# Kernel optimization log

Hardware: AMD Instinct MI355X
Metric: run time of the kernel (lower is better)

The kernel has to match this reference:

```python
import jax, jax.numpy as jnp
import numpy as np

N, E, F, K, T = 100000, 1600000, 64, 3, 2
EPS = 1e-5


def gcn_norm(row, col, edge_weight, num_nodes):
    # symmetric normalization WITHOUT self loops (PyG ARMAConv behavior)
    deg = jax.ops.segment_sum(edge_weight, col, num_segments=num_nodes)
    dis = jnp.where(deg > 0, jax.lax.rsqrt(deg), 0.0)
    return dis[row] * edge_weight * dis[col]


def arma_conv(x, row, col, norm, init_w, w, root_w, bias, num_nodes):
    # x: [N, Fin]; init_w: [K, Fin, Fout]; w: [K, T-1, Fout, Fout]
    # root_w: [K, T, Fin, Fout]; bias: [K, T, 1, Fout]
    n_layers = root_w.shape[1]
    out = jnp.einsum('nf,kfo->kno', x, init_w)  # [K, N, Fout]
    for t in range(n_layers):
        if t > 0:
            out = jnp.einsum('kno,kop->knp', out, w[:, t - 1])
        msg = out[:, row, :] * norm[None, :, None]  # [K, E, Fout]
        out = jax.vmap(lambda m: jax.ops.segment_sum(m, col, num_segments=num_nodes))(msg)
        out = out + jnp.einsum('nf,kfo->kno', x, root_w[:, t]) + bias[:, t]
        out = jax.nn.relu(out)  # ARMAConv act between layers and at output
    return out.mean(axis=0)  # mean over stacks -> [N, Fout]


def batchnorm(h, gamma, beta):
    mu = h.mean(axis=0)
    var = h.var(axis=0)
    return gamma * (h - mu) * jax.lax.rsqrt(var + EPS) + beta


def setup_inputs() -> dict:
    key = jax.random.key(0)
    ks = jax.random.split(key, 16)
    inp = {}
    inp['x'] = jax.random.normal(ks[0], (N, F), jnp.float32)
    inp['edge_index'] = jax.random.randint(ks[1], (2, E), 0, N, dtype=jnp.int32)
    inp['weights'] = jax.random.uniform(ks[2], (E,), jnp.float32)
    s = 0.1
    i = 3
    for c in (1, 2, 3):
        inp[f'iw{c}'] = jax.random.normal(ks[i], (K, F, F), jnp.float32) * s; i += 1
        inp[f'w{c}'] = jax.random.normal(ks[i], (K, T - 1, F, F), jnp.float32) * s; i += 1
        inp[f'rw{c}'] = jax.random.normal(ks[i], (K, T, F, F), jnp.float32) * s; i += 1
        inp[f'b{c}'] = jnp.zeros((K, T, 1, F), jnp.float32)
        inp[f'g{c}'] = jnp.ones((F,), jnp.float32)
        inp[f'be{c}'] = jnp.zeros((F,), jnp.float32)
    return inp


def reference(x, edge_index, weights,
              iw1, w1, rw1, b1, g1, be1,
              iw2, w2, rw2, b2, g2, be2,
              iw3, w3, rw3, b3, g3, be3):
    num_nodes = x.shape[0]
    row, col = edge_index[0], edge_index[1]
    norm = gcn_norm(row, col, weights, num_nodes)
    h = arma_conv(x, row, col, norm, iw1, w1, rw1, b1, num_nodes)
    h = jax.nn.relu(batchnorm(h, g1, be1))
    h = arma_conv(h, row, col, norm, iw2, w2, rw2, b2, num_nodes)
    h = jax.nn.relu(batchnorm(h, g2, be2))
    h = arma_conv(h, row, col, norm, iw3, w3, rw3, b3, num_nodes)
    h = jax.nn.relu(batchnorm(h, g3, be3))
    return h
```

## Files before the change

### kernel.cpp

```cpp
#include <hip/hip_runtime.h>

#define NN 100000
#define NE 1600000
#define FD 64
#define KK 3
#define NF (NN*FD)
#define KNF (KK*NF)
#define EPSBN 1e-5f
#define SBLK ((NN + 255) / 256)
#define DEGSCALE 262144.0f

typedef unsigned short ushort;
typedef unsigned int uint;
typedef __attribute__((ext_vector_type(8))) short short8;
typedef __attribute__((ext_vector_type(4))) float f32x4;

__device__ inline float bf2f(ushort u) { return __uint_as_float((unsigned)u << 16); }
__device__ inline unsigned pk_bf16(float a, float b) {
  unsigned ua = __float_as_uint(a); ua += 0x7FFF + ((ua >> 16) & 1);
  unsigned ub = __float_as_uint(b); ub += 0x7FFF + ((ub >> 16) & 1);
  return (ua >> 16) | (ub & 0xFFFF0000u);
}
__device__ inline ushort f2bf(float v) {
  unsigned u = __float_as_uint(v); u += 0x7FFF + ((u >> 16) & 1);
  return (ushort)(u >> 16);
}

__global__ void k_degcnt(const int* __restrict__ col, const float* __restrict__ w,
                         unsigned long long* __restrict__ dc) {
  int e = blockIdx.x * 256 + threadIdx.x;
  if (e < NE) {
    unsigned fx = __float2uint_rn(w[e] * DEGSCALE);
    atomicAdd(&dc[col[e]], (1ULL << 32) | (unsigned long long)fx);
  }
}

__global__ __launch_bounds__(256) void k_sblk(const unsigned long long* __restrict__ dc,
                                              float* __restrict__ dis, int* __restrict__ cnt,
                                              int* __restrict__ part) {
  int i = blockIdx.x * 256 + threadIdx.x;
  int v = 0;
  if (i < NN) {
    unsigned long long u = dc[i];
    float d = (float)(unsigned)u * (1.0f / DEGSCALE);
    dis[i] = d > 0.f ? rsqrtf(d) : 0.f;
    v = (int)(u >> 32);
    cnt[i] = v;
  }
#pragma unroll
  for (int off = 32; off; off >>= 1) v += __shfl_down(v, off);
  __shared__ int ws[4];
  if ((threadIdx.x & 63) == 0) ws[threadIdx.x >> 6] = v;
  __syncthreads();
  if (threadIdx.x == 0) part[blockIdx.x] = ws[0] + ws[1] + ws[2] + ws[3];
}

__global__ __launch_bounds__(512) void k_sscan(const int* __restrict__ part,
                                               int* __restrict__ base) {
  __shared__ int ls[512];
  int tid = threadIdx.x;
  int v = (tid < SBLK) ? part[tid] : 0;
  ls[tid] = v;
  __syncthreads();
  for (int off = 1; off < 512; off <<= 1) {
    int u = (tid >= off) ? ls[tid - off] : 0;
    __syncthreads();
    ls[tid] += u;
    __syncthreads();
  }
  base[tid] = tid ? ls[tid - 1] : 0;
}

__global__ __launch_bounds__(256) void k_sfin(const int* __restrict__ cnt,
                                              const int* __restrict__ base,
                                              int* __restrict__ rowstart,
                                              int* __restrict__ cursor) {
  __shared__ int ls[256];
  int i = blockIdx.x * 256 + threadIdx.x;
  int v = (i < NN) ? cnt[i] : 0;
  ls[threadIdx.x] = v;
  __syncthreads();
  for (int off = 1; off < 256; off <<= 1) {
    int u = (threadIdx.x >= off) ? ls[threadIdx.x - off] : 0;
    __syncthreads();
    ls[threadIdx.x] += u;
    __syncthreads();
  }
  int excl = base[blockIdx.x] + ls[threadIdx.x] - v;
  if (i < NN) {
    rowstart[i] = excl;
    cursor[i] = excl;
    if (i == NN - 1) rowstart[NN] = excl + v;
  }
}

__global__ void k_place(const int* __restrict__ row, const int* __restrict__ col,
                        const float* __restrict__ w, const float* __restrict__ dis,
                        int* __restrict__ cursor, int2* __restrict__ edges) {
  int e = blockIdx.x * 256 + threadIdx.x;
  if (e >= NE) return;
  int r = row[e], c = col[e];
  float nm = dis[r] * w[e] * dis[c];
  int p = atomicAdd(&cursor[c], 1);
  edges[p] = make_int2(r, __float_as_int(nm));
}

__global__ __launch_bounds__(64) void k_wfrag(const float* __restrict__ iw,
                                              const float* __restrict__ w,
                                              const float* __restrict__ rw,
                                              uint4* __restrict__ frag) {
  int m = blockIdx.x;
  int which = m / 3, k = m % 3;
  const float* src;
  if (which == 0) src = iw + k * 4096;
  else if (which == 1) src = w + k * 4096;
  else if (which == 2) src = rw + k * 8192;
  else src = rw + k * 8192 + 4096;
  int sub = blockIdx.y;
  int ks = sub & 1, ct = sub >> 1;
  int l = threadIdx.x;
  int r0 = ks * 32 + (l >> 4) * 8;
  int c = ct * 16 + (l & 15);
  uint4 o;
  o.x = pk_bf16(src[(r0 + 0) * 64 + c], src[(r0 + 1) * 64 + c]);
  o.y = pk_bf16(src[(r0 + 2) * 64 + c], src[(r0 + 3) * 64 + c]);
  o.z = pk_bf16(src[(r0 + 4) * 64 + c], src[(r0 + 5) * 64 + c]);
  o.w = pk_bf16(src[(r0 + 6) * 64 + c], src[(r0 + 7) * 64 + c]);
  frag[(m * 8 + sub) * 64 + l] = o;
}

__global__ void k_tobf(const float* __restrict__ in, ushort* __restrict__ out) {
  long i = ((long)blockIdx.x * 256 + threadIdx.x) * 4;
  float4 v = *(const float4*)(in + i);
  uint2 u;
  u.x = pk_bf16(v.x, v.y);
  u.y = pk_bf16(v.z, v.w);
  *(uint2*)(out + i) = u;
}

template <bool SAME>
__global__ __launch_bounds__(256) void k_gemm2m(
    const ushort* __restrict__ inA,
    const ushort* __restrict__ inB,
    const uint4* __restrict__ wfA,
    const uint4* __restrict__ wfB,
    ushort* __restrict__ outA, ushort* __restrict__ outB) {
  const int k = blockIdx.y;
  const int wv = threadIdx.x >> 6;
  const int l = threadIdx.x & 63;
  const int lg = l >> 4;
  const int lr = l & 15;
  short8 fA[4][2], fB[4][2];
#pragma unroll
  for (int ct = 0; ct < 4; ++ct)
#pragma unroll
    for (int ks = 0; ks < 2; ++ks) {
      fA[ct][ks] = *(const short8*)&wfA[(k * 8 + ct * 2 + ks) * 64 + l];
      fB[ct][ks] = *(const short8*)&wfB[(k * 8 + ct * 2 + ks) * 64 + l];
    }
  const ushort* srcA = SAME ? inB : (inA + (long)k * NF);
  const int bb = blockIdx.x * 256;
  for (int rt = 0; rt < 4; ++rt) {
    const int tb = bb + rt * 64 + wv * 16;
    int ra = tb + lr; if (ra >= NN) ra = NN - 1;
    const long ao = (long)ra * 64 + lg * 8;
    short8 a0 = *(const short8*)(srcA + ao);
    short8 a1 = *(const short8*)(srcA + ao + 32);
#pragma unroll
    for (int ct = 0; ct < 4; ++ct) {
      f32x4 acc = {0.f, 0.f, 0.f, 0.f};
      acc = __builtin_amdgcn_mfma_f32_16x16x32_bf16(a0, fA[ct][0], acc, 0, 0, 0);
      acc = __builtin_amdgcn_mfma_f32_16x16x32_bf16(a1, fA[ct][1], acc, 0, 0, 0);
      const int f = ct * 16 + lr;
      ushort* op = outA + (long)(tb + lg * 4) * 192 + k * 64 + f;
#pragma unroll
      for (int r = 0; r < 4; ++r)
        if (tb + lg * 4 + r < NN) op[(long)r * 192] = f2bf(acc[r]);
    }
    short8 b0, b1;
    if (SAME) { b0 = a0; b1 = a1; }
    else {
      b0 = *(const short8*)(inB + ao);
      b1 = *(const short8*)(inB + ao + 32);
    }
#pragma unroll
    for (int ct = 0; ct < 4; ++ct) {
      f32x4 acc = {0.f, 0.f, 0.f, 0.f};
      acc = __builtin_amdgcn_mfma_f32_16x16x32_bf16(b0, fB[ct][0], acc, 0, 0, 0);
      acc = __builtin_amdgcn_mfma_f32_16x16x32_bf16(b1, fB[ct][1], acc, 0, 0, 0);
      const int f = ct * 16 + lr;
      ushort* op = outB + (long)k * NF + (long)(tb + lg * 4) * 64 + f;
#pragma unroll
      for (int r = 0; r < 4; ++r)
        if (tb + lg * 4 + r < NN) op[(long)r * 64] = f2bf(acc[r]);
    }
  }
}

#define GSTEP4(EV) do { \
  int2 _e = (EV); \
  float _m = __int_as_float(_e.y); \
  const uint2* _p = (const uint2*)(Abf + (long)_e.x * 192) + fi; \
  uint2 _u0 = _p[0], _u1 = _p[16], _u2 = _p[32]; \
  a00 = fmaf(bf2f((ushort)_u0.x), _m, a00); a01 = fmaf(bf2f((ushort)(_u0.x >> 16)), _m, a01); \
  a02 = fmaf(bf2f((ushort)_u0.y), _m, a02); a03 = fmaf(bf2f((ushort)(_u0.y >> 16)), _m, a03); \
  a10 = fmaf(bf2f((ushort)_u1.x), _m, a10); a11 = fmaf(bf2f((ushort)(_u1.x >> 16)), _m, a11); \
  a12 = fmaf(bf2f((ushort)_u1.y), _m, a12); a13 = fmaf(bf2f((ushort)(_u1.y >> 16)), _m, a13); \
  a20 = fmaf(bf2f((ushort)_u2.x), _m, a20); a21 = fmaf(bf2f((ushort)(_u2.x >> 16)), _m, a21); \
  a22 = fmaf(bf2f((ushort)_u2.y), _m, a22); a23 = fmaf(bf2f((ushort)(_u2.y >> 16)), _m, a23); \
} while (0)

#define RED2(v) do { (v) += __shfl_xor((v), 16); (v) += __shfl_xor((v), 32); } while (0)

template <int MODE>
__global__ __launch_bounds__(256) void k_gather(const int* __restrict__ rowstart,
                                                const int2* __restrict__ edges,
                                                const ushort* __restrict__ Abf,
                                                const ushort* __restrict__ Broot,
                                                ushort* __restrict__ y0,
                                                float* __restrict__ hm,
                                                const float* __restrict__ bias, int t) {
  int wave = threadIdx.x >> 6;
  int lane = threadIdx.x & 63;
  int grp = lane >> 4;
  int fi = lane & 15;
  int n = blockIdx.x * 4 + wave;
  if (n >= NN) return;
  int s = rowstart[n], e = rowstart[n + 1];
  float a00 = 0.f, a01 = 0.f, a02 = 0.f, a03 = 0.f;
  float a10 = 0.f, a11 = 0.f, a12 = 0.f, a13 = 0.f;
  float a20 = 0.f, a21 = 0.f, a22 = 0.f, a23 = 0.f;
  int j = s;
  for (; j + 8 <= e; j += 8) {
    GSTEP4(edges[j + grp]);
    GSTEP4(edges[j + 4 + grp]);
  }
  if (j + 4 <= e) { GSTEP4(edges[j + grp]); j += 4; }
  if (j < e) {
    int idx = j + grp;
    int2 ee = edges[idx < e ? idx : (e - 1)];
    if (idx >= e) ee.y = 0;
    GSTEP4(ee);
  }
  RED2(a00); RED2(a01); RED2(a02); RED2(a03);
  RED2(a10); RED2(a11); RED2(a12); RED2(a13);
  RED2(a20); RED2(a21); RED2(a22); RED2(a23);

  long o4 = (long)n * 64 + 4 * fi;
  if (MODE == 0) {
    if (grp < 3) {
      float4 bb = *(const float4*)(bias + (grp * 2 + t) * 64 + 4 * fi);
      uint2 ru = *(const uint2*)(Broot + (long)grp * NF + o4);
      float aX, aY, aZ, aW;
      if (grp == 0)      { aX = a00; aY = a01; aZ = a02; aW = a03; }
      else if (grp == 1) { aX = a10; aY = a11; aZ = a12; aW = a13; }
      else               { aX = a20; aY = a21; aZ = a22; aW = a23; }
      float rx = fmaxf(bf2f((ushort)ru.x)         + aX + bb.x, 0.f);
      float ry = fmaxf(bf2f((ushort)(ru.x >> 16)) + aY + bb.y, 0.f);
      float rz = fmaxf(bf2f((ushort)ru.y)         + aZ + bb.z, 0.f);
      float rw = fmaxf(bf2f((ushort)(ru.y >> 16)) + aW + bb.w, 0.f);
      uint2 ou;
      ou.x = pk_bf16(rx, ry);
      ou.y = pk_bf16(rz, rw);
      *(uint2*)(y0 + (long)grp * NF + o4) = ou;
    }
  } else {
    if (grp == 0) {
      uint2 r0 = *(const uint2*)(Broot + o4);
      uint2 r1 = *(const uint2*)(Broot + NF + o4);
      uint2 r2 = *(const uint2*)(Broot + 2L * NF + o4);
      float4 c0 = *(const float4*)(bias + (0 * 2 + t) * 64 + 4 * fi);
      float4 c1 = *(const float4*)(bias + (1 * 2 + t) * 64 + 4 * fi);
      float4 c2 = *(const float4*)(bias + (2 * 2 + t) * 64 + 4 * fi);
      float4 r;
      r.x = (fmaxf(bf2f((ushort)r0.x) + a00 + c0.x, 0.f) +
             fmaxf(bf2f((ushort)r1.x) + a10 + c1.x, 0.f) +
             fmaxf(bf2f((ushort)r2.x) + a20 + c2.x, 0.f)) * (1.f / 3.f);
      r.y = (fmaxf(bf2f((ushort)(r0.x >> 16)) + a01 + c0.y, 0.f) +
             fmaxf(bf2f((ushort)(r1.x >> 16)) + a11 + c1.y, 0.f) +
             fmaxf(bf2f((ushort)(r2.x >> 16)) + a21 + c2.y, 0.f)) * (1.f / 3.f);
      r.z = (fmaxf(bf2f((ushort)r0.y) + a02 + c0.z, 0.f) +
             fmaxf(bf2f((ushort)r1.y) + a12 + c1.z, 0.f) +
             fmaxf(bf2f((ushort)r2.y) + a22 + c2.z, 0.f)) * (1.f / 3.f);
      r.w = (fmaxf(bf2f((ushort)(r0.y >> 16)) + a03 + c0.w, 0.f) +
             fmaxf(bf2f((ushort)(r1.y >> 16)) + a13 + c1.w, 0.f) +
             fmaxf(bf2f((ushort)(r2.y >> 16)) + a23 + c2.w, 0.f)) * (1.f / 3.f);
      *(float4*)(hm + o4) = r;
    }
  }
}

__global__ __launch_bounds__(256) void k_bnstats(const float* __restrict__ h,
                                                 float* __restrict__ sum,
                                                 float* __restrict__ sq) {
  int f = threadIdx.x & 63, g = threadIdx.x >> 6;
  float s = 0.f, s2 = 0.f;
  for (int n = blockIdx.x * 4 + g; n < NN; n += gridDim.x * 4) {
    float v = h[(long)n * 64 + f];
    s += v; s2 += v * v;
  }
  __shared__ float ls[512];
  ls[threadIdx.x] = s;
  ls[256 + threadIdx.x] = s2;
  __syncthreads();
  if (threadIdx.x < 64) {
    float ts  = ls[f] + ls[64 + f] + ls[128 + f] + ls[192 + f];
    float ts2 = ls[256 + f] + ls[320 + f] + ls[384 + f] + ls[448 + f];
    atomicAdd(&sum[f], ts);
    atomicAdd(&sq[f], ts2);
  }
}

template <bool FINAL>
__global__ void k_bnfin(const float* __restrict__ h, const float* __restrict__ sum,
                        const float* __restrict__ sq, const float* __restrict__ gam,
                        const float* __restrict__ bet,
                        float* __restrict__ outf, ushort* __restrict__ outbf) {
  long i4 = (long)blockIdx.x * 256 + threadIdx.x;
  if (i4 >= (long)NF / 4) return;
  long i = i4 * 4;
  int f = (int)(i & 63);
  float4 v = *(const float4*)(h + i);
  float o[4] = {v.x, v.y, v.z, v.w};
  float r[4];
#pragma unroll
  for (int j = 0; j < 4; ++j) {
    int fj = f + j;
    float mu = sum[fj] * (1.f / NN);
    float var = sq[fj] * (1.f / NN) - mu * mu;
    float inv = rsqrtf(var + EPSBN);
    float y = gam[fj] * (o[j] - mu) * inv + bet[fj];
    r[j] = fmaxf(y, 0.f);
  }
  if (FINAL) {
    float4 ov = {r[0], r[1], r[2], r[3]};
    *(float4*)(outf + i) = ov;
  } else {
    uint2 u;
    u.x = pk_bf16(r[0], r[1]);
    u.y = pk_bf16(r[2], r[3]);
    *(uint2*)(outbf + i) = u;
  }
}

extern "C" void kernel_launch(void* const* d_in, const int* in_sizes, int n_in,
                              void* d_out, int out_size, void* d_ws, size_t ws_size,
                              hipStream_t stream) {
  const float* x   = (const float*)d_in[0];
  const int*   ei  = (const int*)d_in[1];
  const float* wts = (const float*)d_in[2];
  const int* row = ei;
  const int* col = ei + NE;

  unsigned long long* dc = (unsigned long long*)d_ws;
  uint4* wfrag    = (uint4*)((int*)d_ws + 2 * NN);
  int2*  edges    = (int2*)((int*)wfrag + 73728);
  int*   cnt      = (int*)edges + 2 * NE;
  int*   rowstart = cnt + NN;
  int*   cursor   = rowstart + NN + 4;
  float* dis      = (float*)(cursor + NN);
  float* hm       = dis + NN;
  ushort* xbf     = (ushort*)(hm + NF);
  ushort* Bbf     = xbf + NF;
  ushort* Y0bf    = Bbf + KNF;
  ushort* AbfM    = Y0bf + KNF;
  float* bns      = (float*)(AbfM + (long)NN * 192);
  int*   part     = (int*)(bns + 128);
  int*   pbase    = part + 512;

  hipMemsetAsync(dc, 0, NN * sizeof(unsigned long long), stream);
  int eb = (NE + 255) / 256;
  k_degcnt<<<eb, 256, 0, stream>>>(col, wts, dc);
  k_sblk<<<SBLK, 256, 0, stream>>>(dc, dis, cnt, part);
  k_sscan<<<1, 512, 0, stream>>>(part, pbase);
  k_sfin<<<SBLK, 256, 0, stream>>>(cnt, pbase, rowstart, cursor);
  k_place<<<eb, 256, 0, stream>>>(row, col, wts, dis, cursor, edges);
  for (int L = 0; L < 3; ++L) {
    k_wfrag<<<dim3(12, 8), 64, 0, stream>>>((const float*)d_in[3 + 6 * L],
                                            (const float*)d_in[4 + 6 * L],
                                            (const float*)d_in[5 + 6 * L],
                                            wfrag + (long)L * 6144);
  }
  k_tobf<<<NF / 4 / 256, 256, 0, stream>>>(x, xbf);

  dim3 gg((NN + 255) / 256, KK);
  int gatherBlocks = (NN + 3) / 4;
  int nfBlocks = NF / 4 / 256;

  for (int layer = 0; layer < 3; ++layer) {
    const float* bs = (const float*)d_in[6 + 6 * layer];
    const float* gm = (const float*)d_in[7 + 6 * layer];
    const float* bt = (const float*)d_in[8 + 6 * layer];
    const uint4* wfL = wfrag + (long)layer * 6144;
    k_gemm2m<true><<<gg, 256, 0, stream>>>((const ushort*)0, xbf,
                                           wfL + 0 * 1536, wfL + 2 * 1536, AbfM, Bbf);
    k_gather<0><<<gatherBlocks, 256, 0, stream>>>(rowstart, edges, AbfM, Bbf, Y0bf, hm, bs, 0);
    k_gemm2m<false><<<gg, 256, 0, stream>>>(Y0bf, xbf,
                                            wfL + 1 * 1536, wfL + 3 * 1536, AbfM, Bbf);
    k_gather<1><<<gatherBlocks, 256, 0, stream>>>(rowstart, edges, AbfM, Bbf, Y0bf, hm, bs, 1);
    hipMemsetAsync(bns, 0, 2 * 64 * sizeof(float), stream);
    k_bnstats<<<1024, 256, 0, stream>>>(hm, bns, bns + 64);
    if (layer == 2)
      k_bnfin<true><<<nfBlocks, 256, 0, stream>>>(hm, bns, bns + 64, gm, bt, (float*)d_out, (ushort*)0);
    else
      k_bnfin<false><<<nfBlocks, 256, 0, stream>>>(hm, bns, bns + 64, gm, bt, (float*)0, xbf);
  }
}
```

Baseline: 1.200 ms.

## Aggregate before transform in first ARMA step and fuse root GEMM into gather-output GEMMs

Uses linearity of aggregation, A(XW) = (AX)W, so the first layer step gathers only the 64-wide input once, shared across all stacks, instead of the 192-wide transformed features. A GEMM then applies the init and root weights together with bias and ReLU. The second step gathers the 192-wide y0 and does the W, root, bias, ReLU and stack-mean work in one GEMM kernel, which removes the Broot intermediate. The aim is to cut gather traffic and intermediate writes, at the cost of more MFMA work per GEMM and weight fragments reloaded inside the loop.

Measured after the change: 963.7 us. -19.7%, faster.

```diff
diff --git a/kernel.cpp b/kernel.cpp
--- a/kernel.cpp
+++ b/kernel.cpp
@@ -5,7 +5,6 @@
 #define FD 64
 #define KK 3
 #define NF (NN*FD)
-#define KNF (KK*NF)
 #define EPSBN 1e-5f
 #define SBLK ((NN + 255) / 256)
 #define DEGSCALE 262144.0f
@@ -138,69 +137,53 @@
   *(uint2*)(out + i) = u;
 }
 
-template <bool SAME>
-__global__ __launch_bounds__(256) void k_gemm2m(
-    const ushort* __restrict__ inA,
-    const ushort* __restrict__ inB,
-    const uint4* __restrict__ wfA,
-    const uint4* __restrict__ wfB,
-    ushort* __restrict__ outA, ushort* __restrict__ outB) {
-  const int k = blockIdx.y;
-  const int wv = threadIdx.x >> 6;
-  const int l = threadIdx.x & 63;
-  const int lg = l >> 4;
-  const int lr = l & 15;
-  short8 fA[4][2], fB[4][2];
-#pragma unroll
-  for (int ct = 0; ct < 4; ++ct)
-#pragma unroll
-    for (int ks = 0; ks < 2; ++ks) {
-      fA[ct][ks] = *(const short8*)&wfA[(k * 8 + ct * 2 + ks) * 64 + l];
-      fB[ct][ks] = *(const short8*)&wfB[(k * 8 + ct * 2 + ks) * 64 + l];
-    }
-  const ushort* srcA = SAME ? inB : (inA + (long)k * NF);
-  const int bb = blockIdx.x * 256;
-  for (int rt = 0; rt < 4; ++rt) {
-    const int tb = bb + rt * 64 + wv * 16;
-    int ra = tb + lr; if (ra >= NN) ra = NN - 1;
-    const long ao = (long)ra * 64 + lg * 8;
-    short8 a0 = *(const short8*)(srcA + ao);
-    short8 a1 = *(const short8*)(srcA + ao + 32);
-#pragma unroll
-    for (int ct = 0; ct < 4; ++ct) {
-      f32x4 acc = {0.f, 0.f, 0.f, 0.f};
-      acc = __builtin_amdgcn_mfma_f32_16x16x32_bf16(a0, fA[ct][0], acc, 0, 0, 0);
-      acc = __builtin_amdgcn_mfma_f32_16x16x32_bf16(a1, fA[ct][1], acc, 0, 0, 0);
-      const int f = ct * 16 + lr;
-      ushort* op = outA + (long)(tb + lg * 4) * 192 + k * 64 + f;
-#pragma unroll
-      for (int r = 0; r < 4; ++r)
-        if (tb + lg * 4 + r < NN) op[(long)r * 192] = f2bf(acc[r]);
-    }
-    short8 b0, b1;
-    if (SAME) { b0 = a0; b1 = a1; }
-    else {
-      b0 = *(const short8*)(inB + ao);
-      b1 = *(const short8*)(inB + ao + 32);
-    }
-#pragma unroll
-    for (int ct = 0; ct < 4; ++ct) {
-      f32x4 acc = {0.f, 0.f, 0.f, 0.f};
-      acc = __builtin_amdgcn_mfma_f32_16x16x32_bf16(b0, fB[ct][0], acc, 0, 0, 0);
-      acc = __builtin_amdgcn_mfma_f32_16x16x32_bf16(b1, fB[ct][1], acc, 0, 0, 0);
-      const int f = ct * 16 + lr;
-      ushort* op = outB + (long)k * NF + (long)(tb + lg * 4) * 64 + f;
-#pragma unroll
-      for (int r = 0; r < 4; ++r)
-        if (tb + lg * 4 + r < NN) op[(long)r * 64] = f2bf(acc[r]);
-    }
-  }
-}
-
-#define GSTEP4(EV) do { \
+#define RED2(v) do { (v) += __shfl_xor((v), 16); (v) += __shfl_xor((v), 32); } while (0)
+
+#define G0STEP(EV) do { \
   int2 _e = (EV); \
   float _m = __int_as_float(_e.y); \
-  const uint2* _p = (const uint2*)(Abf + (long)_e.x * 192) + fi; \
+  uint2 _u = ((const uint2*)(xsrc + (long)_e.x * 64))[fi]; \
+  a0 = fmaf(bf2f((ushort)_u.x), _m, a0); a1 = fmaf(bf2f((ushort)(_u.x >> 16)), _m, a1); \
+  a2 = fmaf(bf2f((ushort)_u.y), _m, a2); a3 = fmaf(bf2f((ushort)(_u.y >> 16)), _m, a3); \
+} while (0)
+
+__global__ __launch_bounds__(256) void k_gath0(const int* __restrict__ rowstart,
+                                               const int2* __restrict__ edges,
+                                               const ushort* __restrict__ xsrc,
+                                               ushort* __restrict__ g) {
+  int wave = threadIdx.x >> 6;
+  int lane = threadIdx.x & 63;
+  int grp = lane >> 4;
+  int fi = lane & 15;
+  int n = blockIdx.x * 4 + wave;
+  if (n >= NN) return;
+  int s = rowstart[n], e = rowstart[n + 1];
+  float a0 = 0.f, a1 = 0.f, a2 = 0.f, a3 = 0.f;
+  int j = s;
+  for (; j + 8 <= e; j += 8) {
+    G0STEP(edges[j + grp]);
+    G0STEP(edges[j + 4 + grp]);
+  }
+  if (j + 4 <= e) { G0STEP(edges[j + grp]); j += 4; }
+  if (j < e) {
+    int idx = j + grp;
+    int2 ee = edges[idx < e ? idx : (e - 1)];
+    if (idx >= e) ee.y = 0;
+    G0STEP(ee);
+  }
+  RED2(a0); RED2(a1); RED2(a2); RED2(a3);
+  if (grp == 0) {
+    uint2 o;
+    o.x = pk_bf16(a0, a1);
+    o.y = pk_bf16(a2, a3);
+    *(uint2*)(g + (long)n * 64 + 4 * fi) = o;
+  }
+}
+
+#define G1STEP(EV) do { \
+  int2 _e = (EV); \
+  float _m = __int_as_float(_e.y); \
+  const uint2* _p = (const uint2*)(y0 + (long)_e.x * 192) + fi; \
   uint2 _u0 = _p[0], _u1 = _p[16], _u2 = _p[32]; \
   a00 = fmaf(bf2f((ushort)_u0.x), _m, a00); a01 = fmaf(bf2f((ushort)(_u0.x >> 16)), _m, a01); \
   a02 = fmaf(bf2f((ushort)_u0.y), _m, a02); a03 = fmaf(bf2f((ushort)(_u0.y >> 16)), _m, a03); \
@@ -210,16 +193,10 @@
   a22 = fmaf(bf2f((ushort)_u2.y), _m, a22); a23 = fmaf(bf2f((ushort)(_u2.y >> 16)), _m, a23); \
 } while (0)
 
-#define RED2(v) do { (v) += __shfl_xor((v), 16); (v) += __shfl_xor((v), 32); } while (0)
-
-template <int MODE>
-__global__ __launch_bounds__(256) void k_gather(const int* __restrict__ rowstart,
-                                                const int2* __restrict__ edges,
-                                                const ushort* __restrict__ Abf,
-                                                const ushort* __restrict__ Broot,
-                                                ushort* __restrict__ y0,
-                                                float* __restrict__ hm,
-                                                const float* __restrict__ bias, int t) {
+__global__ __launch_bounds__(256) void k_gath1(const int* __restrict__ rowstart,
+                                               const int2* __restrict__ edges,
+                                               const ushort* __restrict__ y0,
+                                               ushort* __restrict__ G) {
   int wave = threadIdx.x >> 6;
   int lane = threadIdx.x & 63;
   int grp = lane >> 4;
@@ -232,60 +209,122 @@
   float a20 = 0.f, a21 = 0.f, a22 = 0.f, a23 = 0.f;
   int j = s;
   for (; j + 8 <= e; j += 8) {
-    GSTEP4(edges[j + grp]);
-    GSTEP4(edges[j + 4 + grp]);
-  }
-  if (j + 4 <= e) { GSTEP4(edges[j + grp]); j += 4; }
+    G1STEP(edges[j + grp]);
+    G1STEP(edges[j + 4 + grp]);
+  }
+  if (j + 4 <= e) { G1STEP(edges[j + grp]); j += 4; }
   if (j < e) {
     int idx = j + grp;
     int2 ee = edges[idx < e ? idx : (e - 1)];
     if (idx >= e) ee.y = 0;
-    GSTEP4(ee);
+    G1STEP(ee);
   }
   RED2(a00); RED2(a01); RED2(a02); RED2(a03);
   RED2(a10); RED2(a11); RED2(a12); RED2(a13);
   RED2(a20); RED2(a21); RED2(a22); RED2(a23);
-
-  long o4 = (long)n * 64 + 4 * fi;
-  if (MODE == 0) {
-    if (grp < 3) {
-      float4 bb = *(const float4*)(bias + (grp * 2 + t) * 64 + 4 * fi);
-      uint2 ru = *(const uint2*)(Broot + (long)grp * NF + o4);
-      float aX, aY, aZ, aW;
-      if (grp == 0)      { aX = a00; aY = a01; aZ = a02; aW = a03; }
-      else if (grp == 1) { aX = a10; aY = a11; aZ = a12; aW = a13; }
-      else               { aX = a20; aY = a21; aZ = a22; aW = a23; }
-      float rx = fmaxf(bf2f((ushort)ru.x)         + aX + bb.x, 0.f);
-      float ry = fmaxf(bf2f((ushort)(ru.x >> 16)) + aY + bb.y, 0.f);
-      float rz = fmaxf(bf2f((ushort)ru.y)         + aZ + bb.z, 0.f);
-      float rw = fmaxf(bf2f((ushort)(ru.y >> 16)) + aW + bb.w, 0.f);
-      uint2 ou;
-      ou.x = pk_bf16(rx, ry);
-      ou.y = pk_bf16(rz, rw);
-      *(uint2*)(y0 + (long)grp * NF + o4) = ou;
+  if (grp < 3) {
+    float aX, aY, aZ, aW;
+    if (grp == 0)      { aX = a00; aY = a01; aZ = a02; aW = a03; }
+    else if (grp == 1) { aX = a10; aY = a11; aZ = a12; aW = a13; }
+    else               { aX = a20; aY = a21; aZ = a22; aW = a23; }
+    uint2 o;
+    o.x = pk_bf16(aX, aY);
+    o.y = pk_bf16(aZ, aW);
+    *(uint2*)(G + (long)n * 192 + grp * 64 + 4 * fi) = o;
+  }
+}
+
+__global__ __launch_bounds__(256) void k_gemmY0(
+    const ushort* __restrict__ g, const ushort* __restrict__ xbf,
+    const uint4* __restrict__ wfA, const uint4* __restrict__ wfB,
+    const float* __restrict__ bias, ushort* __restrict__ y0) {
+  const int k = blockIdx.y;
+  const int wv = threadIdx.x >> 6;
+  const int l = threadIdx.x & 63;
+  const int lg = l >> 4;
+  const int lr = l & 15;
+  short8 fA[4][2], fB[4][2];
+#pragma unroll
+  for (int ct = 0; ct < 4; ++ct)
+#pragma unroll
+    for (int ks = 0; ks < 2; ++ks) {
+      fA[ct][ks] = *(const short8*)&wfA[(k * 8 + ct * 2 + ks) * 64 + l];
+      fB[ct][ks] = *(const short8*)&wfB[(k * 8 + ct * 2 + ks) * 64 + l];
     }
-  } else {
-    if (grp == 0) {
-      uint2 r0 = *(const uint2*)(Broot + o4);
-      uint2 r1 = *(const uint2*)(Broot + NF + o4);
-      uint2 r2 = *(const uint2*)(Broot + 2L * NF + o4);
-      float4 c0 = *(const float4*)(bias + (0 * 2 + t) * 64 + 4 * fi);
-      float4 c1 = *(const float4*)(bias + (1 * 2 + t) * 64 + 4 * fi);
-      float4 c2 = *(const float4*)(bias + (2 * 2 + t) * 64 + 4 * fi);
-      float4 r;
-      r.x = (fmaxf(bf2f((ushort)r0.x) + a00 + c0.x, 0.f) +
-             fmaxf(bf2f((ushort)r1.x) + a10 + c1.x, 0.f) +
-             fmaxf(bf2f((ushort)r2.x) + a20 + c2.x, 0.f)) * (1.f / 3.f);
-      r.y = (fmaxf(bf2f((ushort)(r0.x >> 16)) + a01 + c0.y, 0.f) +
-             fmaxf(bf2f((ushort)(r1.x >> 16)) + a11 + c1.y, 0.f) +
-             fmaxf(bf2f((ushort)(r2.x >> 16)) + a21 + c2.y, 0.f)) * (1.f / 3.f);
-      r.z = (fmaxf(bf2f((ushort)r0.y) + a02 + c0.z, 0.f) +
-             fmaxf(bf2f((ushort)r1.y) + a12 + c1.z, 0.f) +
-             fmaxf(bf2f((ushort)r2.y) + a22 + c2.z, 0.f)) * (1.f / 3.f);
-      r.w = (fmaxf(bf2f((ushort)(r0.y >> 16)) + a03 + c0.w, 0.f) +
-             fmaxf(bf2f((ushort)(r1.y >> 16)) + a13 + c1.w, 0.f) +
-             fmaxf(bf2f((ushort)(r2.y >> 16)) + a23 + c2.w, 0.f)) * (1.f / 3.f);
-      *(float4*)(hm + o4) = r;
+  const int bb = blockIdx.x * 256;
+  for (int rt = 0; rt < 4; ++rt) {
+    const int tb = bb + rt * 64 + wv * 16;
+    int ra = tb + lr; if (ra >= NN) ra = NN - 1;
+    const long ao = (long)ra * 64 + lg * 8;
+    short8 a0 = *(const short8*)(g + ao);
+    short8 a1 = *(const short8*)(g + ao + 32);
+    short8 b0 = *(const short8*)(xbf + ao);
+    short8 b1 = *(const short8*)(xbf + ao + 32);
+#pragma unroll
+    for (int ct = 0; ct < 4; ++ct) {
+      f32x4 acc = {0.f, 0.f, 0.f, 0.f};
+      acc = __builtin_amdgcn_mfma_f32_16x16x32_bf16(a0, fA[ct][0], acc, 0, 0, 0);
+      acc = __builtin_amdgcn_mfma_f32_16x16x32_bf16(a1, fA[ct][1], acc, 0, 0, 0);
+      acc = __builtin_amdgcn_mfma_f32_16x16x32_bf16(b0, fB[ct][0], acc, 0, 0, 0);
+      acc = __builtin_amdgcn_mfma_f32_16x16x32_bf16(b1, fB[ct][1], acc, 0, 0, 0);
+      const int f = ct * 16 + lr;
+      const float bv = bias[(k * 2 + 0) * 64 + f];
+      ushort* op = y0 + (long)(tb + lg * 4) * 192 + k * 64 + f;
+#pragma unroll
+      for (int r = 0; r < 4; ++r)
+        if (tb + lg * 4 + r < NN) op[(long)r * 192] = f2bf(fmaxf(acc[r] + bv, 0.f));
+    }
+  }
+}
+
+__global__ __launch_bounds__(256) void k_gemmY1(
+    const ushort* __restrict__ G, const ushort* __restrict__ xbf,
+    const uint4* __restrict__ wfW, const uint4* __restrict__ wfR,
+    const float* __restrict__ bias, float* __restrict__ hm) {
+  const int wv = threadIdx.x >> 6;
+  const int l = threadIdx.x & 63;
+  const int lg = l >> 4;
+  const int lr = l & 15;
+  const int bb = blockIdx.x * 256;
+  for (int rt = 0; rt < 4; ++rt) {
+    const int tb = bb + rt * 64 + wv * 16;
+    int ra = tb + lr; if (ra >= NN) ra = NN - 1;
+    const long xo = (long)ra * 64 + lg * 8;
+    short8 ax0 = *(const short8*)(xbf + xo);
+    short8 ax1 = *(const short8*)(xbf + xo + 32);
+    f32x4 m0 = {0.f, 0.f, 0.f, 0.f}, m1 = m0, m2 = m0, m3 = m0;
+#pragma unroll
+    for (int k = 0; k < 3; ++k) {
+      const long go = (long)ra * 192 + k * 64 + lg * 8;
+      short8 g0 = *(const short8*)(G + go);
+      short8 g1 = *(const short8*)(G + go + 32);
+      const int k8 = k * 8;
+#define YCT(CT, M) { \
+      short8 fw0 = *(const short8*)&wfW[(k8 + CT * 2 + 0) * 64 + l]; \
+      short8 fw1 = *(const short8*)&wfW[(k8 + CT * 2 + 1) * 64 + l]; \
+      short8 fr0 = *(const short8*)&wfR[(k8 + CT * 2 + 0) * 64 + l]; \
+      short8 fr1 = *(const short8*)&wfR[(k8 + CT * 2 + 1) * 64 + l]; \
+      f32x4 acc = {0.f, 0.f, 0.f, 0.f}; \
+      acc = __builtin_amdgcn_mfma_f32_16x16x32_bf16(g0, fw0, acc, 0, 0, 0); \
+      acc = __builtin_amdgcn_mfma_f32_16x16x32_bf16(g1, fw1, acc, 0, 0, 0); \
+      acc = __builtin_amdgcn_mfma_f32_16x16x32_bf16(ax0, fr0, acc, 0, 0, 0); \
+      acc = __builtin_amdgcn_mfma_f32_16x16x32_bf16(ax1, fr1, acc, 0, 0, 0); \
+      float bv = bias[(k * 2 + 1) * 64 + CT * 16 + lr]; \
+      M[0] += fmaxf(acc[0] + bv, 0.f); M[1] += fmaxf(acc[1] + bv, 0.f); \
+      M[2] += fmaxf(acc[2] + bv, 0.f); M[3] += fmaxf(acc[3] + bv, 0.f); }
+      YCT(0, m0) YCT(1, m1) YCT(2, m2) YCT(3, m3)
+#undef YCT
+    }
+    const int rb = tb + lg * 4;
+#pragma unroll
+    for (int r = 0; r < 4; ++r) {
+      if (rb + r < NN) {
+        float* hp = hm + (long)(rb + r) * 64 + lr;
+        hp[0]  = m0[r] * (1.f / 3.f);
+        hp[16] = m1[r] * (1.f / 3.f);
+        hp[32] = m2[r] * (1.f / 3.f);
+        hp[48] = m3[r] * (1.f / 3.f);
+      }
     }
   }
 }
@@ -361,10 +400,10 @@
   float* dis      = (float*)(cursor + NN);
   float* hm       = dis + NN;
   ushort* xbf     = (ushort*)(hm + NF);
-  ushort* Bbf     = xbf + NF;
-  ushort* Y0bf    = Bbf + KNF;
-  ushort* AbfM    = Y0bf + KNF;
-  float* bns      = (float*)(AbfM + (long)NN * 192);
+  ushort* g       = xbf + NF;
+  ushort* y0      = g + NF;
+  ushort* Gb      = y0 + (long)NN * 192;
+  float* bns      = (float*)(Gb + (long)NN * 192);
   int*   part     = (int*)(bns + 128);
   int*   pbase    = part + 512;
 
@@ -383,8 +422,7 @@
   }
   k_tobf<<<NF / 4 / 256, 256, 0, stream>>>(x, xbf);
 
-  dim3 gg((NN + 255) / 256, KK);
-  int gatherBlocks = (NN + 3) / 4;
+  int gB = (NN + 3) / 4;
   int nfBlocks = NF / 4 / 256;
 
   for (int layer = 0; layer < 3; ++layer) {
@@ -392,12 +430,11 @@
     const float* gm = (const float*)d_in[7 + 6 * layer];
     const float* bt = (const float*)d_in[8 + 6 * layer];
     const uint4* wfL = wfrag + (long)layer * 6144;
-    k_gemm2m<true><<<gg, 256, 0, stream>>>((const ushort*)0, xbf,
-                                           wfL + 0 * 1536, wfL + 2 * 1536, AbfM, Bbf);
-    k_gather<0><<<gatherBlocks, 256, 0, stream>>>(rowstart, edges, AbfM, Bbf, Y0bf, hm, bs, 0);
-    k_gemm2m<false><<<gg, 256, 0, stream>>>(Y0bf, xbf,
-                                            wfL + 1 * 1536, wfL + 3 * 1536, AbfM, Bbf);
-    k_gather<1><<<gatherBlocks, 256, 0, stream>>>(rowstart, edges, AbfM, Bbf, Y0bf, hm, bs, 1);
+
+    k_gath0<<<gB, 256, 0, stream>>>(rowstart, edges, xbf, g);
+    k_gemmY0<<<dim3(SBLK, 3), 256, 0, stream>>>(g, xbf, wfL, wfL + 2 * 1536, bs, y0);
+    k_gath1<<<gB, 256, 0, stream>>>(rowstart, edges, y0, Gb);
+    k_gemmY1<<<SBLK, 256, 0, stream>>>(Gb, xbf, wfL + 1 * 1536, wfL + 3 * 1536, bs, hm);
     hipMemsetAsync(bns, 0, 2 * 64 * sizeof(float), stream);
     k_bnstats<<<1024, 256, 0, stream>>>(hm, bns, bns + 64);
     if (layer == 2)
```
